# Kernel tuning notes

Measured on AMD Instinct MI355X. Metric: run time of the kernel, lower is better.

The kernel has to match this reference:

```python
import jax, jax.numpy as jnp
import numpy as np

B, T, C = 2, 2048, 768
N_HEADS = 12
HEAD = C // N_HEADS


def setup_inputs() -> dict:
    key = jax.random.key(0)
    k1, k2, k3 = jax.random.split(key, 3)
    x = jax.random.normal(k1, (B, T, C), dtype=jnp.float32)
    # torch Linear weights: [out_features, in_features]
    W_attn = jax.random.normal(k2, (3 * C, C), dtype=jnp.float32) * 0.02
    W_proj = jax.random.normal(k3, (C, C), dtype=jnp.float32) * 0.02
    return {"x": x, "W_attn": W_attn, "W_proj": W_proj}


def reference(x, W_attn, W_proj):
    b, t, c = x.shape
    qkv = jnp.einsum('btc,oc->bto', x, W_attn)  # [B,T,3C]
    q, k, v = jnp.split(qkv, 3, axis=-1)
    # [B, H, T, D]
    q = q.reshape(b, t, N_HEADS, HEAD).transpose(0, 2, 1, 3)
    k = k.reshape(b, t, N_HEADS, HEAD).transpose(0, 2, 1, 3)
    v = v.reshape(b, t, N_HEADS, HEAD).transpose(0, 2, 1, 3)
    scale = 1.0 / jnp.sqrt(jnp.asarray(HEAD, dtype=x.dtype))
    wei = jnp.einsum('bhqd,bhkd->bhqk', q, k) * scale  # [B,H,T,T]
    causal = jnp.tril(jnp.ones((t, t), dtype=bool))
    wei = jnp.where(causal[None, None], wei, jnp.asarray(-jnp.inf, dtype=wei.dtype))
    wei = jax.nn.softmax(wei, axis=-1)  # dropout p=0 -> identity
    out = jnp.einsum('bhqk,bhkd->bhqd', wei, v)
    out = out.transpose(0, 2, 1, 3).reshape(b, t, c)
    out = jnp.einsum('btc,oc->bto', out, W_proj)
    return out
```

## Files before the change

kernel.cpp:

```cpp
#include <hip/hip_runtime.h>

#define T_DIM 2048
#define C_DIM 768
#define NH    12
#define HD    64
#define KDIM  768
#define JOBS_PER_XCD 96

typedef __attribute__((ext_vector_type(8))) short short8;
typedef __attribute__((ext_vector_type(4))) float f32x4;
typedef unsigned short u16;

__device__ __forceinline__ u16 f2bf(float f) {
    unsigned int u = __builtin_bit_cast(unsigned int, f);
    u = (u + 0x7fffu + ((u >> 16) & 1u)) >> 16;
    return (u16)u;
}
__device__ __forceinline__ unsigned int cvtpk(float a, float b) {
    unsigned int r;
    asm("v_cvt_pk_bf16_f32 %0, %1, %2" : "=v"(r) : "v"(a), "v"(b));
    return r;
}
__device__ __forceinline__ void gload16(const u16* g, u16* l) {
    __builtin_amdgcn_global_load_lds(
        (const __attribute__((address_space(1))) unsigned int*)g,
        (__attribute__((address_space(3))) unsigned int*)l, 16, 0, 0);
}

#define NX  (4096 * 768)
#define NWA (2304 * 768)
#define NWP (768 * 768)
#define TOT4 ((NX + NWA + NWP) / 4)

__global__ __launch_bounds__(256) void convert_all(
    const float* __restrict__ x, const float* __restrict__ wa,
    const float* __restrict__ wp, u16* __restrict__ xb,
    u16* __restrict__ wab, u16* __restrict__ wpb, int* __restrict__ counters)
{
    if (blockIdx.x == 0 && threadIdx.x < 8) counters[threadIdx.x * 16] = 0;
    for (int i4 = blockIdx.x * 256 + threadIdx.x; i4 < TOT4; i4 += gridDim.x * 256) {
        int i = i4 * 4;
        const float* src; u16* dst; int off;
        if (i < NX)            { src = x;  dst = xb;  off = i; }
        else if (i < NX + NWA) { src = wa; dst = wab; off = i - NX; }
        else                   { src = wp; dst = wpb; off = i - NX - NWA; }
        float4 v = *(const float4*)&src[off];
        ushort4 o;
        o.x = f2bf(v.x); o.y = f2bf(v.y); o.z = f2bf(v.z); o.w = f2bf(v.w);
        *(ushort4*)&dst[off] = o;
    }
}

__global__ __launch_bounds__(256) void gemm_qkv(
    const u16* __restrict__ A, const u16* __restrict__ Wt,
    u16* __restrict__ qb, u16* __restrict__ kb, u16* __restrict__ vtb)
{
    __shared__ __align__(16) u16 AsL[2][128][32];
    __shared__ __align__(16) u16 BsL[2][128][32];

    const int tid = threadIdx.x;
    const int orig = blockIdx.x;
    const int wg = (orig & 7) * 72 + (orig >> 3);
    const int bm = (wg / 18) * 128;
    const int bn = (wg % 18) * 128;

    const int w = tid >> 6, l = tid & 63;
    const int wr = (w >> 1) * 64, wc = (w & 1) * 64;
    const int lrow = l & 15, lg = l >> 4;
    const int lr4 = l >> 2, lc4 = l & 3;

    f32x4 acc[4][4];
    const f32x4 zero4 = {0.f, 0.f, 0.f, 0.f};
#pragma unroll
    for (int mi = 0; mi < 4; ++mi)
#pragma unroll
        for (int ni = 0; ni < 4; ++ni) acc[mi][ni] = zero4;

    auto STAGE = [&](int buf, int k0) {
#pragma unroll
        for (int i = 0; i < 2; ++i) {
            const int rb = w * 32 + i * 16;
            const int row = rb + lr4;
            const int sc = (lc4 ^ (row & 3)) * 8;
            gload16(&A [(size_t)(bm + row) * KDIM + k0 + sc], &AsL[buf][rb][0]);
            gload16(&Wt[(size_t)(bn + row) * KDIM + k0 + sc], &BsL[buf][rb][0]);
        }
    };

    int cur = 0;
    STAGE(0, 0);
    for (int k0 = 0; k0 < KDIM; k0 += 32) {
        __syncthreads();
        if (k0 + 32 < KDIM) STAGE(cur ^ 1, k0 + 32);

        short8 af[4], bf[4];
#pragma unroll
        for (int mi = 0; mi < 4; ++mi)
            af[mi] = *(const short8*)&AsL[cur][wr + mi * 16 + lrow][(lg ^ (lrow & 3)) * 8];
#pragma unroll
        for (int ni = 0; ni < 4; ++ni)
            bf[ni] = *(const short8*)&BsL[cur][wc + ni * 16 + lrow][(lg ^ (lrow & 3)) * 8];
#pragma unroll
        for (int mi = 0; mi < 4; ++mi)
#pragma unroll
            for (int ni = 0; ni < 4; ++ni)
                acc[mi][ni] = __builtin_amdgcn_mfma_f32_16x16x32_bf16(
                    af[mi], bf[ni], acc[mi][ni], 0, 0, 0);
        cur ^= 1;
    }

#pragma unroll
    for (int ni = 0; ni < 4; ++ni) {
        const int colbase = bn + wc + ni * 16;
        const int which = colbase / C_DIM;
        const int h = (colbase % C_DIM) / HD;
        const int d = (colbase % HD) + lrow;
        const float qs = (which == 0) ? 0.18033688011112042f : 1.0f;
#pragma unroll
        for (int mi = 0; mi < 4; ++mi) {
            const int t0 = bm + wr + mi * 16 + lg * 4;
            const int bb2 = t0 >> 11, tt = t0 & 2047;
            const size_t bhoff = (size_t)(bb2 * NH + h);
            if (which == 2) {
                ushort4 pv;
                pv.x = f2bf(acc[mi][ni][0]); pv.y = f2bf(acc[mi][ni][1]);
                pv.z = f2bf(acc[mi][ni][2]); pv.w = f2bf(acc[mi][ni][3]);
                *(ushort4*)&vtb[(bhoff * HD + d) * T_DIM + tt] = pv;
            } else {
                u16* dst = (which == 0) ? qb : kb;
#pragma unroll
                for (int jj = 0; jj < 4; ++jj)
                    dst[(bhoff * T_DIM + tt + jj) * HD + d] = f2bf(acc[mi][ni][jj] * qs);
            }
        }
    }
}

__global__ __launch_bounds__(256) void gemm_proj(
    const u16* __restrict__ A, const u16* __restrict__ Wt,
    float* __restrict__ dense)
{
    __shared__ __align__(16) u16 As[64][40];
    __shared__ __align__(16) u16 Bs[128][40];

    const int tid = threadIdx.x;
    const int orig = blockIdx.x;
    const int wg = (orig & 7) * 48 + (orig >> 3);
    const int bm = (wg / 6) * 64, bn = (wg % 6) * 128;

    const int w = tid >> 6, l = tid & 63;
    const int wr = (w >> 1) * 32, wc = (w & 1) * 64;
    const int lrow = l & 15, lg = l >> 4;

    const int srow = tid >> 2;
    const int scol = (tid & 3) * 8;

    f32x4 acc[2][4];
    const f32x4 zero4 = {0.f, 0.f, 0.f, 0.f};
#pragma unroll
    for (int mi = 0; mi < 2; ++mi)
#pragma unroll
        for (int ni = 0; ni < 4; ++ni) acc[mi][ni] = zero4;

    uint4 ra0 = *(const uint4*)&A [(size_t)(bm + srow)      * KDIM + scol];
    uint4 rb0 = *(const uint4*)&Wt[(size_t)(bn + srow)      * KDIM + scol];
    uint4 rb1 = *(const uint4*)&Wt[(size_t)(bn + 64 + srow) * KDIM + scol];

    for (int k0 = 0; k0 < KDIM; k0 += 32) {
        __syncthreads();
        *(uint4*)&As[srow][scol]      = ra0;
        *(uint4*)&Bs[srow][scol]      = rb0;
        *(uint4*)&Bs[64 + srow][scol] = rb1;
        __syncthreads();

        if (k0 + 32 < KDIM) {
            ra0 = *(const uint4*)&A [(size_t)(bm + srow)      * KDIM + k0 + 32 + scol];
            rb0 = *(const uint4*)&Wt[(size_t)(bn + srow)      * KDIM + k0 + 32 + scol];
            rb1 = *(const uint4*)&Wt[(size_t)(bn + 64 + srow) * KDIM + k0 + 32 + scol];
        }

        short8 af[2], bf[4];
#pragma unroll
        for (int mi = 0; mi < 2; ++mi)
            af[mi] = *(const short8*)&As[wr + mi * 16 + lrow][lg * 8];
#pragma unroll
        for (int ni = 0; ni < 4; ++ni)
            bf[ni] = *(const short8*)&Bs[wc + ni * 16 + lrow][lg * 8];
#pragma unroll
        for (int mi = 0; mi < 2; ++mi)
#pragma unroll
            for (int ni = 0; ni < 4; ++ni)
                acc[mi][ni] = __builtin_amdgcn_mfma_f32_16x16x32_bf16(
                    af[mi], bf[ni], acc[mi][ni], 0, 0, 0);
    }

#pragma unroll
    for (int ni = 0; ni < 4; ++ni) {
        const int col = bn + wc + ni * 16 + lrow;
#pragma unroll
        for (int mi = 0; mi < 2; ++mi) {
            const int m0 = bm + wr + mi * 16 + lg * 4;
#pragma unroll
            for (int jj = 0; jj < 4; ++jj)
                dense[(size_t)(m0 + jj) * C_DIM + col] = acc[mi][ni][jj];
        }
    }
}

__global__ __launch_bounds__(256, 2) void attn_mfma(
    const u16* __restrict__ q, const u16* __restrict__ k,
    const u16* __restrict__ vt, u16* __restrict__ aw, int* __restrict__ counters)
{
    __shared__ __align__(16) u16 KsL [2][128][64];
    __shared__ __align__(16) u16 VtsL[2][64][128];
    __shared__ __align__(16) u16 Ps  [4][16][72];
    __shared__ int job_s;

    const int tid = threadIdx.x, w = tid >> 6, l = tid & 63;
    const int lrow = l & 15, lg = l >> 4;
    const int lr8 = l >> 3, lc8 = l & 7;
    const int lr16 = l >> 4, lc16 = l & 15;
    const int xcdi = blockIdx.x & 7;
    const f32x4 zero4 = {0.f, 0.f, 0.f, 0.f};

    for (;;) {
        __syncthreads();
        if (tid == 0) job_s = atomicAdd(&counters[xcdi * 16], 1);
        __syncthreads();
        const int j = job_s;
        if (j >= JOBS_PER_XCD) break;

        const int qt = 31 - (j / 3);
        const int bh = xcdi * 3 + (j - (j / 3) * 3);
        const int bb = bh / NH, hh = bh % NH;
        const int qbase = qt * 64 + w * 16;
        const int qg = qbase + lrow;

        const u16* Qp = q  + (size_t)bh * T_DIM * HD;
        const u16* Kp = k  + (size_t)bh * T_DIM * HD;
        const u16* Vp = vt + (size_t)bh * HD * T_DIM;

        const short8 aq0 = *(const short8*)&Qp[(size_t)(qbase + lrow) * HD + lg * 8];
        const short8 aq1 = *(const short8*)&Qp[(size_t)(qbase + lrow) * HD + 32 + lg * 8];

        f32x4 o[4];
#pragma unroll
        for (int n = 0; n < 4; ++n) o[n] = zero4;
        float l_run = 0.0f;

        auto STAGE = [&](int buf, int kk0) {
#pragma unroll
            for (int i = 0; i < 4; ++i) {
                const int rb = w * 32 + i * 8;
                const int row = rb + lr8;
                gload16(&Kp[(size_t)(kk0 + row) * HD + ((lc8 ^ (row & 7)) * 8)],
                        &KsL[buf][rb][0]);
            }
#pragma unroll
            for (int i = 0; i < 4; ++i) {
                const int db = w * 16 + i * 4;
                const int d = db + lr16;
                gload16(&Vp[(size_t)d * T_DIM + kk0 + ((lc16 ^ (d & 15)) * 8)],
                        &VtsL[buf][db][0]);
            }
        };

        auto PROCESS = [&](f32x4* s, int sub, int kk0, bool masked) {
            if (masked) {
#pragma unroll
                for (int n = 0; n < 4; ++n)
#pragma unroll
                    for (int jj = 0; jj < 4; ++jj)
                        if (kk0 + sub * 64 + n * 16 + lg * 4 + jj > qg)
                            s[n][jj] = -3.0e38f;
            }
#pragma unroll
            for (int n = 0; n < 4; ++n)
#pragma unroll
                for (int jj = 0; jj < 4; ++jj)
                    s[n][jj] = exp2f(s[n][jj]);
            f32x4 a2 = (s[0] + s[1]) + (s[2] + s[3]);
            l_run += (a2[0] + a2[1]) + (a2[2] + a2[3]);
#pragma unroll
            for (int n = 0; n < 4; ++n) {
                uint2 pr;
                pr.x = cvtpk(s[n][0], s[n][1]);
                pr.y = cvtpk(s[n][2], s[n][3]);
                *(uint2*)&Ps[w][lrow][n * 16 + lg * 4] = pr;
            }
            const short8 ap0 = *(const short8*)&Ps[w][lrow][lg * 8];
            const short8 ap1 = *(const short8*)&Ps[w][lrow][32 + lg * 8];
            const int cur = (kk0 >> 7) & 1;
#pragma unroll
            for (int n = 0; n < 4; ++n) {
                const int row = n * 16 + lrow;
                const short8 bv0 = *(const short8*)
                    &VtsL[cur][row][((sub * 8 + lg) ^ lrow) * 8];
                const short8 bv1 = *(const short8*)
                    &VtsL[cur][row][((sub * 8 + 4 + lg) ^ lrow) * 8];
                o[n] = __builtin_amdgcn_mfma_f32_16x16x32_bf16(ap0, bv0, o[n], 0, 0, 0);
                o[n] = __builtin_amdgcn_mfma_f32_16x16x32_bf16(ap1, bv1, o[n], 0, 0, 0);
            }
        };

        const int nkt = qt / 2 + 1;
        int cur = 0;
        STAGE(0, 0);
        for (int kt = 0; kt < nkt; ++kt) {
            const int kk0 = kt * 128;
            __syncthreads();
            if (kt + 1 < nkt) STAGE(cur ^ 1, kk0 + 128);

            const bool last = (kt == nkt - 1);
            const int nsub = (last && (qt & 1) == 0) ? 1 : 2;

            f32x4 s0[4], s1[4];
#pragma unroll
            for (int n = 0; n < 4; ++n) {
                const int row = n * 16 + lrow;
                const short8 kf0 = *(const short8*)&KsL[cur][row][((lg)     ^ (lrow & 7)) * 8];
                const short8 kf1 = *(const short8*)&KsL[cur][row][((lg + 4) ^ (lrow & 7)) * 8];
                s0[n] = __builtin_amdgcn_mfma_f32_16x16x32_bf16(kf0, aq0, zero4, 0, 0, 0);
                s0[n] = __builtin_amdgcn_mfma_f32_16x16x32_bf16(kf1, aq1, s0[n], 0, 0, 0);
            }
            if (nsub == 2) {
#pragma unroll
                for (int n = 0; n < 4; ++n) {
                    const int row = 64 + n * 16 + lrow;
                    const short8 kf0 = *(const short8*)&KsL[cur][row][((lg)     ^ (lrow & 7)) * 8];
                    const short8 kf1 = *(const short8*)&KsL[cur][row][((lg + 4) ^ (lrow & 7)) * 8];
                    s1[n] = __builtin_amdgcn_mfma_f32_16x16x32_bf16(kf0, aq0, zero4, 0, 0, 0);
                    s1[n] = __builtin_amdgcn_mfma_f32_16x16x32_bf16(kf1, aq1, s1[n], 0, 0, 0);
                }
            }

            PROCESS(s0, 0, kk0, last && nsub == 1);
            if (nsub == 2) PROCESS(s1, 1, kk0, last);

            cur ^= 1;
        }

        float rs = l_run;
        rs += __shfl_xor(rs, 16);
        rs += __shfl_xor(rs, 32);
#pragma unroll
        for (int jj = 0; jj < 4; ++jj) {
            const float lj = __shfl(rs, lg * 4 + jj);
            const float inv = 1.0f / lj;
            const size_t m = (size_t)bb * T_DIM + qbase + lg * 4 + jj;
#pragma unroll
            for (int n = 0; n < 4; ++n)
                aw[m * C_DIM + hh * HD + n * 16 + lrow] = f2bf(o[n][jj] * inv);
        }
    }
}

extern "C" void kernel_launch(void* const* d_in, const int* in_sizes, int n_in,
                              void* d_out, int out_size, void* d_ws, size_t ws_size,
                              hipStream_t stream) {
    const float* x      = (const float*)d_in[0];
    const float* W_attn = (const float*)d_in[1];
    const float* W_proj = (const float*)d_in[2];
    float* out = (float*)d_out;

    char* ws = (char*)d_ws;
    u16* xb  = (u16*)ws;                       ws += (size_t)NX * 2;
    u16* wab = (u16*)ws;                       ws += (size_t)NWA * 2;
    u16* wpb = (u16*)ws;                       ws += (size_t)NWP * 2;
    u16* qb  = (u16*)ws;                       ws += (size_t)24 * T_DIM * HD * 2;
    u16* kb  = (u16*)ws;                       ws += (size_t)24 * T_DIM * HD * 2;
    u16* vtb = (u16*)ws;                       ws += (size_t)24 * T_DIM * HD * 2;
    u16* awb = (u16*)ws;                       ws += (size_t)4096 * C_DIM * 2;
    int* cnt = (int*)ws;

    convert_all<<<2048, 256, 0, stream>>>(x, W_attn, W_proj, xb, wab, wpb, cnt);

    gemm_qkv<<<576, 256, 0, stream>>>(xb, wab, qb, kb, vtb);

    attn_mfma<<<512, 256, 0, stream>>>(qb, kb, vtb, awb, cnt);

    gemm_proj<<<384, 256, 0, stream>>>(awb, wpb, out);
}
```

Measured before the change: 85.53 us.

## Load V fragments directly from global and double K tile to 256 rows

The attention kernel no longer stages V^T through LDS. Each wave now loads its V fragments straight from global memory into registers for each 64-key sub-block, and the freed LDS is used to double the K tile to 256 rows per stage, which halves the number of block barriers. The loop is restructured into a per-64-key sub-loop with s_setprio raised around the MFMA sections. The cost is uncached, strided global loads of V that each wave issues redundantly, which may add latency and memory traffic.

```diff
diff --git a/kernel.cpp b/kernel.cpp
--- a/kernel.cpp
+++ b/kernel.cpp
@@ -211,15 +211,13 @@
     const u16* __restrict__ q, const u16* __restrict__ k,
     const u16* __restrict__ vt, u16* __restrict__ aw, int* __restrict__ counters)
 {
-    __shared__ __align__(16) u16 KsL [2][128][64];
-    __shared__ __align__(16) u16 VtsL[2][64][128];
-    __shared__ __align__(16) u16 Ps  [4][16][72];
+    __shared__ __align__(16) u16 KsL[2][256][64];
+    __shared__ __align__(16) u16 Ps [4][16][72];
     __shared__ int job_s;
 
     const int tid = threadIdx.x, w = tid >> 6, l = tid & 63;
     const int lrow = l & 15, lg = l >> 4;
     const int lr8 = l >> 3, lc8 = l & 7;
-    const int lr16 = l >> 4, lc16 = l & 15;
     const int xcdi = blockIdx.x & 7;
     const f32x4 zero4 = {0.f, 0.f, 0.f, 0.f};
 
@@ -250,93 +248,82 @@
 
         auto STAGE = [&](int buf, int kk0) {
 #pragma unroll
-            for (int i = 0; i < 4; ++i) {
-                const int rb = w * 32 + i * 8;
+            for (int i = 0; i < 8; ++i) {
+                const int rb = w * 64 + i * 8;
                 const int row = rb + lr8;
                 gload16(&Kp[(size_t)(kk0 + row) * HD + ((lc8 ^ (row & 7)) * 8)],
                         &KsL[buf][rb][0]);
             }
-#pragma unroll
-            for (int i = 0; i < 4; ++i) {
-                const int db = w * 16 + i * 4;
-                const int d = db + lr16;
-                gload16(&Vp[(size_t)d * T_DIM + kk0 + ((lc16 ^ (d & 15)) * 8)],
-                        &VtsL[buf][db][0]);
-            }
         };
 
-        auto PROCESS = [&](f32x4* s, int sub, int kk0, bool masked) {
-            if (masked) {
-#pragma unroll
-                for (int n = 0; n < 4; ++n)
-#pragma unroll
-                    for (int jj = 0; jj < 4; ++jj)
-                        if (kk0 + sub * 64 + n * 16 + lg * 4 + jj > qg)
-                            s[n][jj] = -3.0e38f;
-            }
-#pragma unroll
-            for (int n = 0; n < 4; ++n)
-#pragma unroll
-                for (int jj = 0; jj < 4; ++jj)
-                    s[n][jj] = exp2f(s[n][jj]);
-            f32x4 a2 = (s[0] + s[1]) + (s[2] + s[3]);
-            l_run += (a2[0] + a2[1]) + (a2[2] + a2[3]);
-#pragma unroll
-            for (int n = 0; n < 4; ++n) {
-                uint2 pr;
-                pr.x = cvtpk(s[n][0], s[n][1]);
-                pr.y = cvtpk(s[n][2], s[n][3]);
-                *(uint2*)&Ps[w][lrow][n * 16 + lg * 4] = pr;
-            }
-            const short8 ap0 = *(const short8*)&Ps[w][lrow][lg * 8];
-            const short8 ap1 = *(const short8*)&Ps[w][lrow][32 + lg * 8];
-            const int cur = (kk0 >> 7) & 1;
-#pragma unroll
-            for (int n = 0; n < 4; ++n) {
-                const int row = n * 16 + lrow;
-                const short8 bv0 = *(const short8*)
-                    &VtsL[cur][row][((sub * 8 + lg) ^ lrow) * 8];
-                const short8 bv1 = *(const short8*)
-                    &VtsL[cur][row][((sub * 8 + 4 + lg) ^ lrow) * 8];
-                o[n] = __builtin_amdgcn_mfma_f32_16x16x32_bf16(ap0, bv0, o[n], 0, 0, 0);
-                o[n] = __builtin_amdgcn_mfma_f32_16x16x32_bf16(ap1, bv1, o[n], 0, 0, 0);
-            }
-        };
-
-        const int nkt = qt / 2 + 1;
+        const int totsub = qt + 1;
+        const int nkt = qt / 4 + 1;
         int cur = 0;
         STAGE(0, 0);
         for (int kt = 0; kt < nkt; ++kt) {
-            const int kk0 = kt * 128;
             __syncthreads();
-            if (kt + 1 < nkt) STAGE(cur ^ 1, kk0 + 128);
-
-            const bool last = (kt == nkt - 1);
-            const int nsub = (last && (qt & 1) == 0) ? 1 : 2;
-
-            f32x4 s0[4], s1[4];
-#pragma unroll
-            for (int n = 0; n < 4; ++n) {
-                const int row = n * 16 + lrow;
-                const short8 kf0 = *(const short8*)&KsL[cur][row][((lg)     ^ (lrow & 7)) * 8];
-                const short8 kf1 = *(const short8*)&KsL[cur][row][((lg + 4) ^ (lrow & 7)) * 8];
-                s0[n] = __builtin_amdgcn_mfma_f32_16x16x32_bf16(kf0, aq0, zero4, 0, 0, 0);
-                s0[n] = __builtin_amdgcn_mfma_f32_16x16x32_bf16(kf1, aq1, s0[n], 0, 0, 0);
+            if (kt + 1 < nkt) STAGE(cur ^ 1, (kt + 1) * 256);
+
+            const int nsl = min(4, totsub - 4 * kt);
+#pragma unroll 4
+            for (int sub = 0; sub < nsl; ++sub) {
+                const int gsub = 4 * kt + sub;
+                const int kb = gsub * 64;
+                const bool masked = (gsub == qt);
+
+                short8 vf[8];
+#pragma unroll
+                for (int n = 0; n < 4; ++n) {
+                    vf[2 * n]     = *(const short8*)&Vp[(size_t)(n * 16 + lrow) * T_DIM + kb + lg * 8];
+                    vf[2 * n + 1] = *(const short8*)&Vp[(size_t)(n * 16 + lrow) * T_DIM + kb + 32 + lg * 8];
+                }
+
+                f32x4 s[4];
+                __builtin_amdgcn_s_setprio(1);
+#pragma unroll
+                for (int n = 0; n < 4; ++n) {
+                    const int row = sub * 64 + n * 16 + lrow;
+                    const short8 kf0 = *(const short8*)&KsL[cur][row][((lg)     ^ (row & 7)) * 8];
+                    const short8 kf1 = *(const short8*)&KsL[cur][row][((lg + 4) ^ (row & 7)) * 8];
+                    s[n] = __builtin_amdgcn_mfma_f32_16x16x32_bf16(kf0, aq0, zero4, 0, 0, 0);
+                    s[n] = __builtin_amdgcn_mfma_f32_16x16x32_bf16(kf1, aq1, s[n], 0, 0, 0);
+                }
+                __builtin_amdgcn_s_setprio(0);
+
+                if (masked) {
+#pragma unroll
+                    for (int n = 0; n < 4; ++n)
+#pragma unroll
+                        for (int jj = 0; jj < 4; ++jj)
+                            if (kb + n * 16 + lg * 4 + jj > qg) s[n][jj] = -3.0e38f;
+                }
+
+#pragma unroll
+                for (int n = 0; n < 4; ++n)
+#pragma unroll
+                    for (int jj = 0; jj < 4; ++jj)
+                        s[n][jj] = exp2f(s[n][jj]);
+                f32x4 a2 = (s[0] + s[1]) + (s[2] + s[3]);
+                l_run += (a2[0] + a2[1]) + (a2[2] + a2[3]);
+
+#pragma unroll
+                for (int n = 0; n < 4; ++n) {
+                    uint2 pr;
+                    pr.x = cvtpk(s[n][0], s[n][1]);
+                    pr.y = cvtpk(s[n][2], s[n][3]);
+                    *(uint2*)&Ps[w][lrow][n * 16 + lg * 4] = pr;
+                }
+                const short8 ap0 = *(const short8*)&Ps[w][lrow][lg * 8];
+                const short8 ap1 = *(const short8*)&Ps[w][lrow][32 + lg * 8];
+
+                __builtin_amdgcn_s_setprio(1);
+#pragma unroll
+                for (int n = 0; n < 4; ++n) {
+                    o[n] = __builtin_amdgcn_mfma_f32_16x16x32_bf16(ap0, vf[2 * n],     o[n], 0, 0, 0);
+                    o[n] = __builtin_amdgcn_mfma_f32_16x16x32_bf16(ap1, vf[2 * n + 1], o[n], 0, 0, 0);
+                }
+                __builtin_amdgcn_s_setprio(0);
             }
-            if (nsub == 2) {
-#pragma unroll
-                for (int n = 0; n < 4; ++n) {
-                    const int row = 64 + n * 16 + lrow;
-                    const short8 kf0 = *(const short8*)&KsL[cur][row][((lg)     ^ (lrow & 7)) * 8];
-                    const short8 kf1 = *(const short8*)&KsL[cur][row][((lg + 4) ^ (lrow & 7)) * 8];
-                    s1[n] = __builtin_amdgcn_mfma_f32_16x16x32_bf16(kf0, aq0, zero4, 0, 0, 0);
-                    s1[n] = __builtin_amdgcn_mfma_f32_16x16x32_bf16(kf1, aq1, s1[n], 0, 0, 0);
-                }
-            }
-
-            PROCESS(s0, 0, kk0, last && nsub == 1);
-            if (nsub == 2) PROCESS(s1, 1, kk0, last);
-
             cur ^= 1;
         }
 
```

After: 114.5 us. 33.8% more time.
